# Kernel tuning notes

Hardware: AMD Instinct MI355X
Metric: run time of the kernel (lower is better)

## Reference

```python
import jax, jax.numpy as jnp
import numpy as np

D = 32   # input_dim == all hidden dims
L = 4    # number of GeneralizedRelationalConv layers
R = 36   # num_relation (incl. inverse relations)


def _bellmanford(edge_index, edge_type, h_index, r_index, num_nodes,
                 query_emb, rel_W, rel_b, conv_W, conv_b):
    """NBFNet Bellman-Ford pass: relation-conditioned conv with PNA aggregation."""
    B = r_index.shape[0]
    N = num_nodes
    E = edge_type.shape[0]
    d = query_emb.shape[1]

    query = query_emb[r_index]                                   # [B, d]
    # boundary condition: indicator embedding at the head node
    boundary = jnp.zeros((B, N, d), jnp.float32).at[jnp.arange(B), h_index].add(query)

    src, dst = edge_index[0], edge_index[1]
    # augment every node with a self-loop carrying the boundary message
    idx_aug = jnp.concatenate([dst, jnp.arange(N)])              # [E + N]
    deg = jax.ops.segment_sum(jnp.ones(E + N, jnp.float32), idx_aug, num_segments=N)  # >= 1
    dlog = jnp.log(deg)
    scale = dlog / jnp.mean(dlog)
    # PNA degree scalers: identity / amplification / attenuation
    scales = jnp.stack([jnp.ones_like(scale), scale, 1.0 / jnp.clip(scale, 1e-2)], axis=-1)  # [N, 3]

    x = boundary
    for l in range(L):
        # dependent relation embeddings: linear projection of the query
        rel = (query @ rel_W[l].T + rel_b[l]).reshape(B, R, d)   # [B, R, d]
        # distmult message: gather source state, modulate by edge relation
        msg = x[:, src, :] * rel[:, edge_type, :]                # [B, E, d]
        msg = jnp.concatenate([msg, boundary], axis=1)           # [B, E+N, d] incl. self-loops

        def agg(m):  # segment stats over destination nodes
            s = jax.ops.segment_sum(m, idx_aug, num_segments=N)
            sq = jax.ops.segment_sum(m * m, idx_aug, num_segments=N)
            mx = jax.ops.segment_max(m, idx_aug, num_segments=N)
            mn = jax.ops.segment_min(m, idx_aug, num_segments=N)
            return s, sq, mx, mn

        s, sq, mx, mn = jax.vmap(agg)(msg)                       # each [B, N, d]
        mean = s / deg[:, None]
        sq_mean = sq / deg[:, None]
        std = jnp.sqrt(jnp.clip(sq_mean - mean * mean, 1e-6))
        feats = jnp.stack([mean, mx, mn, std], axis=-1).reshape(B, N, 4 * d)
        update = (feats[..., None] * scales[None, :, None, :]).reshape(B, N, 12 * d)
        # combine: linear over cat(input, pna_update) then ReLU
        x = jax.nn.relu(jnp.concatenate([x, update], axis=-1) @ conv_W[l].T + conv_b[l])

    node_query = jnp.broadcast_to(query[:, None, :], (B, N, d))
    return jnp.concatenate([x, node_query], axis=-1)             # [B, N, 2d]


def setup_inputs() -> dict:
    key = jax.random.key(0)
    ks = jax.random.split(key, 10)
    N, E, B, K = 20000, 200000, 4, 32
    return {
        "edge_index": jax.random.randint(ks[0], (2, E), 0, N),
        "edge_type": jax.random.randint(ks[1], (E,), 0, R),
        "h_index": jax.random.randint(ks[2], (B,), 0, N),
        "t_index": jax.random.randint(ks[3], (B, K), 0, N),
        "r_index": jax.random.randint(ks[4], (B,), 0, R),
        "num_nodes": N,
        "query_emb": jax.random.normal(ks[5], (R, D), jnp.float32) * 0.1,
        "rel_W": jax.random.normal(ks[6], (L, R * D, D), jnp.float32) * 0.1,
        "rel_b": jnp.zeros((L, R * D), jnp.float32),
        "conv_W": jax.random.normal(ks[7], (L, D, 13 * D), jnp.float32) * 0.05,
        "conv_b": jnp.zeros((L, D), jnp.float32),
        "mlp_W1": jax.random.normal(ks[8], (2 * D, 2 * D), jnp.float32) * 0.1,
        "mlp_b1": jnp.zeros((2 * D,), jnp.float32),
        "mlp_W2": jax.random.normal(ks[9], (1, 2 * D), jnp.float32) * 0.1,
        "mlp_b2": jnp.zeros((1,), jnp.float32),
    }


def reference(edge_index, edge_type, h_index, t_index, r_index, num_nodes,
              query_emb, rel_W, rel_b, conv_W, conv_b,
              mlp_W1, mlp_b1, mlp_W2, mlp_b2):
    feature = _bellmanford(edge_index, edge_type, h_index, r_index, num_nodes,
                           query_emb, rel_W, rel_b, conv_W, conv_b)
    B = h_index.shape[0]
    f_t = feature[jnp.arange(B)[:, None], t_index]               # [B, K, 2d]
    h = jax.nn.relu(f_t @ mlp_W1.T + mlp_b1)
    score = (h @ mlp_W2.T + mlp_b2)[..., 0]                      # [B, K]
    return score
```

## Files before the change

kernel.cpp:

```cpp
#include <hip/hip_runtime.h>
#include <hip/hip_bf16.h>

#define N_NODES 20000
#define N_EDGES 200000
#define BB 4
#define KK 32
#define DD 32
#define RR 36
#define LL 4
#define NCHUNKS (N_NODES / 16)
#define NBLK 79

constexpr size_t OFF_X0   = 0;
constexpr size_t OFF_X1   = OFF_X0 + (size_t)BB * N_NODES * DD;
constexpr size_t OFF_RP   = OFF_X1 + (size_t)BB * N_NODES * DD;
constexpr size_t OFF_CUR  = OFF_RP + 20032;
constexpr size_t OFF_ES   = OFF_CUR + N_NODES;
constexpr size_t OFF_DEG  = OFF_ES + N_EDGES;
constexpr size_t OFF_SC   = OFF_DEG + N_NODES;
constexpr size_t OFF_INV  = OFF_SC + N_NODES;
constexpr size_t OFF_BS   = OFF_INV + N_NODES;
constexpr size_t OFF_BL   = OFF_BS + 128;
constexpr size_t OFF_BO   = OFF_BL + 128;
constexpr size_t OFF_MEAN = OFF_BO + 128;
constexpr size_t OFF_REL  = OFF_MEAN + 16;
constexpr size_t OFF_PW   = OFF_REL + (size_t)LL * RR * BB * DD;
constexpr size_t OFF_F    = OFF_PW + (size_t)LL * 4 * 3328;


__global__ void k_init(const int* __restrict__ h_index, const int* __restrict__ r_index,
                       const float* __restrict__ query_emb, float* __restrict__ x0,
                       int* __restrict__ cursor) {
    int i = blockIdx.x * blockDim.x + threadIdx.x;
    int stride = gridDim.x * blockDim.x;
    for (int t = i; t < N_NODES; t += stride) cursor[t] = 0;
    for (int t = i; t < BB * N_NODES * DD; t += stride) {
        int b = t & 3; int d = (t >> 2) & 31; int n = t >> 7;
        float v = 0.f;
        if (n == h_index[b]) v = query_emb[r_index[b] * DD + d];
        x0[t] = v;
    }
}

__global__ void k_hist(const int* __restrict__ ei, int* __restrict__ cursor) {
    int e = blockIdx.x * blockDim.x + threadIdx.x;
    if (e < N_EDGES) atomicAdd(&cursor[ei[N_EDGES + e]], 1);
}

__global__ void k_part(const int* __restrict__ cursor, int* __restrict__ bsum,
                       float* __restrict__ blog) {
    __shared__ int si[256];
    __shared__ float sf2[256];
    int tid = threadIdx.x;
    int i = blockIdx.x * 256 + tid;
    int v = (i < N_NODES) ? cursor[i] : 0;
    float lg = (i < N_NODES) ? logf((float)(v + 1)) : 0.f;
    si[tid] = v; sf2[tid] = lg;
    __syncthreads();
    for (int off = 128; off > 0; off >>= 1) {
        if (tid < off) { si[tid] += si[tid + off]; sf2[tid] += sf2[tid + off]; }
        __syncthreads();
    }
    if (tid == 0) { bsum[blockIdx.x] = si[0]; blog[blockIdx.x] = sf2[0]; }
}

__global__ void k_scan2(const int* __restrict__ bsum, const float* __restrict__ blog,
                        int* __restrict__ boff, float* __restrict__ meanw) {
    __shared__ int si[128];
    __shared__ float sf2[128];
    int t = threadIdx.x;
    int v = (t < NBLK) ? bsum[t] : 0;
    float lg = (t < NBLK) ? blog[t] : 0.f;
    si[t] = v; sf2[t] = lg;
    __syncthreads();
    for (int off = 1; off < 128; off <<= 1) {
        int tv = (t >= off) ? si[t - off] : 0;
        float tf = (t >= off) ? sf2[t - off] : 0.f;
        __syncthreads();
        si[t] += tv; sf2[t] += tf;
        __syncthreads();
    }
    if (t < NBLK) boff[t] = si[t] - v;
    if (t == 127) meanw[0] = sf2[127] / (float)N_NODES;
}

__global__ void k_final(int* __restrict__ cursor, int* __restrict__ row_ptr,
                        const int* __restrict__ boff, const float* __restrict__ meanw,
                        float* __restrict__ rdeg, float* __restrict__ scale,
                        float* __restrict__ invs) {
    __shared__ int si[256];
    int tid = threadIdx.x;
    int i = blockIdx.x * 256 + tid;
    int v = (i < N_NODES) ? cursor[i] : 0;
    si[tid] = v;
    __syncthreads();
    for (int off = 1; off < 256; off <<= 1) {
        int tv = (tid >= off) ? si[tid - off] : 0;
        __syncthreads();
        si[tid] += tv;
        __syncthreads();
    }
    int rp = boff[blockIdx.x] + si[tid] - v;
    if (i < N_NODES) {
        row_ptr[i] = rp;
        cursor[i] = rp;
        float dg = (float)(v + 1);
        float sc = logf(dg) / meanw[0];
        rdeg[i] = 1.f / dg;
        scale[i] = sc;
        invs[i] = 1.f / fmaxf(sc, 0.01f);
    }
    if (i == 0) row_ptr[N_NODES] = N_EDGES;
}

__global__ void k_scatter(const int* __restrict__ ei, const int* __restrict__ et,
                          int* __restrict__ cursor, int* __restrict__ es) {
    int e = blockIdx.x * blockDim.x + threadIdx.x;
    if (e < N_EDGES) {
        int dnode = ei[N_EDGES + e];
        int p = atomicAdd(&cursor[dnode], 1);
        es[p] = ei[e] | (et[e] << 16);
    }
}

__global__ void k_prep_w(const float* __restrict__ query_emb, const int* __restrict__ r_index,
                         const float* __restrict__ rel_W, const float* __restrict__ rel_b,
                         const float* __restrict__ conv_W,
                         float* __restrict__ rel_all, float* __restrict__ pw) {
    int i = blockIdx.x * blockDim.x + threadIdx.x;
    const int NREL = LL * BB * RR * DD;
    if (i < NREL) {
        int d = i & 31;
        int ty = (i >> 5) % RR;
        int b = (i / (32 * RR)) & 3;
        int l = i / (32 * RR * BB);
        const float* q = query_emb + r_index[b] * DD;
        const float* w = rel_W + ((size_t)l * RR * DD + ty * DD + d) * DD;
        float acc = rel_b[l * RR * DD + ty * DD + d];
        #pragma unroll
        for (int k2 = 0; k2 < DD; ++k2) acc = fmaf(q[k2], w[k2], acc);
        rel_all[(((size_t)l * RR + ty) * DD + d) * BB + b] = acc;
    } else {
        int i2 = i - NREL;
        if (i2 >= LL * 4 * 3328) return;
        int r = i2 % 3328; int lg2 = i2 / 3328;
        int og = lg2 & 3, l = lg2 >> 2;
        int o, col;
        if (r < 256) { col = r >> 3; o = og * 8 + (r & 7); }
        else {
            int r2 = r - 256;
            int jj = r2 / 96, rem = r2 % 96;
            int pf = rem >> 3;
            o = og * 8 + (rem & 7);
            col = DD + (jj * 4 + pf / 3) * 3 + (pf % 3);
        }
        pw[i2] = conv_W[(size_t)(l * DD + o) * (13 * DD) + col];
    }
}

__launch_bounds__(256, 6)
__global__ void k_gather(const float* __restrict__ xin, float4* __restrict__ Fq,
                         const int* __restrict__ row_ptr, const int* __restrict__ es,
                         const float* __restrict__ rel_l, const float* __restrict__ rdeg,
                         const int* __restrict__ h_index, const int* __restrict__ r_index,
                         const float* __restrict__ query_emb) {
    __shared__ __align__(16) float s_rel[RR * BB * DD];
    const int tid = threadIdx.x;
    {
        const float4* p4 = (const float4*)rel_l;
        float4* s4 = (float4*)s_rel;
        for (int i = tid; i < RR * BB * DD / 4; i += 256) s4[i] = p4[i];
    }
    const int lane = tid & 63;
    const int d = lane & 31;
    const int par = lane >> 5;
    int hb[4]; float qv[4];
    #pragma unroll
    for (int b = 0; b < 4; ++b) {
        hb[b] = h_index[b];
        qv[b] = query_emb[r_index[b] * DD + d];
    }
    __syncthreads();

    const int nwaves = gridDim.x * 4;
    for (int n = blockIdx.x * 4 + (tid >> 6); n < N_NODES; n += nwaves) {
        float sa[4], sq[4], mx[4], mn[4];
        #pragma unroll
        for (int b = 0; b < 4; ++b) {
            float bv = (n == hb[b]) ? qv[b] : 0.f;
            float bs = par ? 0.f : bv;
            sa[b] = bs; sq[b] = bs * bv; mx[b] = bv; mn[b] = bv;
        }
        auto proc = [&](int ee) {
            int pk = es[ee];
            float4 xv = *(const float4*)(xin + ((size_t)(pk & 0xFFFF) * DD + d) * 4);
            float4 rv = *(const float4*)(s_rel + (((pk >> 16) * DD) + d) * 4);
            #pragma unroll
            for (int b = 0; b < 4; ++b) {
                float m = (&xv.x)[b] * (&rv.x)[b];
                sa[b] += m; sq[b] = fmaf(m, m, sq[b]);
                mx[b] = fmaxf(mx[b], m); mn[b] = fminf(mn[b], m);
            }
        };
        int e0 = row_ptr[n], e1 = row_ptr[n + 1];
        int e = e0 + par;
        for (; e + 6 < e1; e += 8) { proc(e); proc(e + 2); proc(e + 4); proc(e + 6); }
        for (; e < e1; e += 2) proc(e);
        #pragma unroll
        for (int b = 0; b < 4; ++b) {
            sa[b] += __shfl_xor(sa[b], 32);
            sq[b] += __shfl_xor(sq[b], 32);
            mx[b] = fmaxf(mx[b], __shfl_xor(mx[b], 32));
            mn[b] = fminf(mn[b], __shfl_xor(mn[b], 32));
        }
        float rd_ = rdeg[n];
        float mean[4], sd[4];
        #pragma unroll
        for (int b = 0; b < 4; ++b) {
            mean[b] = sa[b] * rd_;
            float sm = sq[b] * rd_;
            sd[b] = sqrtf(fmaxf(sm - mean[b] * mean[b], 1e-6f));
        }
        const int chunk = n >> 4, nl = n & 15;
        int tA = nl * 4 + par * 2;
        float4 fA, fB;
        fA.x = par ? mean[2] : mean[0]; fA.y = par ? mx[2] : mx[0];
        fA.z = par ? mn[2] : mn[0];     fA.w = par ? sd[2] : sd[0];
        fB.x = par ? mean[3] : mean[1]; fB.y = par ? mx[3] : mx[1];
        fB.z = par ? mn[3] : mn[1];     fB.w = par ? sd[3] : sd[1];
        Fq[(size_t)(chunk * 32 + d) * 64 + tA] = fA;
        Fq[(size_t)(chunk * 32 + d) * 64 + tA + 1] = fB;
    }
}

__launch_bounds__(256, 6)
__global__ void k_conv(const float* __restrict__ xin, float* __restrict__ xout,
                       const float4* __restrict__ Fq, const float* __restrict__ pw_l,
                       const float* __restrict__ scale, const float* __restrict__ invs,
                       const float* __restrict__ conv_b_l) {
    const int tid = threadIdx.x;
    const int og = __builtin_amdgcn_readfirstlane(tid >> 6);
    const int lane = tid & 63;
    const int chunk = blockIdx.x;
    const float* wxp = pw_l + og * 3328;
    const float* wfp = wxp + 256;

    const int nl2 = lane >> 2, b2 = lane & 3;
    const int n = chunk * 16 + nl2;

    float y0[8], y1[8], y2[8];
    #pragma unroll
    for (int oo = 0; oo < 8; ++oo) {
        y0[oo] = conv_b_l[og * 8 + oo];
        y1[oo] = 0.f;
        y2[oo] = 0.f;
    }

    const float* xb = xin + (size_t)n * 128 + b2;
    #pragma unroll 2
    for (int jg = 0; jg < 8; ++jg) {
        float cxv[4];
        #pragma unroll
        for (int dj = 0; dj < 4; ++dj) cxv[dj] = xb[(jg * 4 + dj) * 4];
        #pragma unroll
        for (int dj = 0; dj < 4; ++dj) {
            const float* wp = wxp + (jg * 4 + dj) * 8;
            #pragma unroll
            for (int oo = 0; oo < 8; ++oo) y0[oo] = fmaf(cxv[dj], wp[oo], y0[oo]);
        }
    }

    float4 fa = Fq[(size_t)(chunk * 32) * 64 + lane];
    #pragma unroll 1
    for (int jj = 0; jj < 32; ++jj) {
        float4 fb = Fq[(size_t)(chunk * 32 + jj + 1) * 64 + lane];
        const float* wp = wfp + jj * 96;
        #pragma unroll
        for (int f = 0; f < 4; ++f) {
            float cv = (&fa.x)[f];
            const float* w8 = wp + f * 24;
            #pragma unroll
            for (int oo = 0; oo < 8; ++oo) y0[oo] = fmaf(cv, w8[oo], y0[oo]);
            #pragma unroll
            for (int oo = 0; oo < 8; ++oo) y1[oo] = fmaf(cv, w8[8 + oo], y1[oo]);
            #pragma unroll
            for (int oo = 0; oo < 8; ++oo) y2[oo] = fmaf(cv, w8[16 + oo], y2[oo]);
        }
        fa = fb;
    }

    float scn = scale[n], ivn = invs[n];
    float* xo = xout + (size_t)n * 128 + b2;
    #pragma unroll
    for (int oo = 0; oo < 8; ++oo) {
        float v = fmaxf(0.f, y0[oo] + scn * y1[oo] + ivn * y2[oo]);
        xo[(og * 8 + oo) * 4] = v;
    }
}

__global__ void k_score(const float* __restrict__ xL, const float* __restrict__ query_emb,
                        const int* __restrict__ r_index, const int* __restrict__ t_index,
                        const float* __restrict__ W1, const float* __restrict__ b1,
                        const float* __restrict__ W2, const float* __restrict__ b2,
                        float* __restrict__ out) {
    int bi = blockIdx.x;
    int b = bi >> 5, kk = bi & 31;
    int j = threadIdx.x;
    __shared__ float sf[64];
    int t = t_index[b * KK + kk];
    float f = (j < DD) ? xL[(size_t)t * 128 + j * 4 + b]
                       : query_emb[r_index[b] * DD + (j - DD)];
    sf[j] = f;
    __syncthreads();
    float acc = b1[j];
    #pragma unroll 8
    for (int i2 = 0; i2 < 64; ++i2) acc = fmaf(sf[i2], W1[j * 64 + i2], acc);
    float h = fmaxf(acc, 0.f);
    float prod = h * W2[j];
    #pragma unroll
    for (int off = 32; off > 0; off >>= 1) prod += __shfl_down(prod, off);
    if (j == 0) out[b * KK + kk] = prod + b2[0];
}

extern "C" void kernel_launch(void* const* d_in, const int* in_sizes, int n_in,
                              void* d_out, int out_size, void* d_ws, size_t ws_size,
                              hipStream_t stream) {
    const int* ei        = (const int*)d_in[0];
    const int* et        = (const int*)d_in[1];
    const int* h_index   = (const int*)d_in[2];
    const int* t_index   = (const int*)d_in[3];
    const int* r_index   = (const int*)d_in[4];
    const float* query_emb = (const float*)d_in[6];
    const float* rel_W   = (const float*)d_in[7];
    const float* rel_b   = (const float*)d_in[8];
    const float* conv_W  = (const float*)d_in[9];
    const float* conv_b  = (const float*)d_in[10];
    const float* W1      = (const float*)d_in[11];
    const float* b1      = (const float*)d_in[12];
    const float* W2      = (const float*)d_in[13];
    const float* b2      = (const float*)d_in[14];

    float* ws = (float*)d_ws;
    float* x0      = ws + OFF_X0;
    float* x1      = ws + OFF_X1;
    int*   row_ptr = (int*)(ws + OFF_RP);
    int*   cursor  = (int*)(ws + OFF_CUR);
    int*   es      = (int*)(ws + OFF_ES);
    float* rdeg    = ws + OFF_DEG;
    float* sc      = ws + OFF_SC;
    float* invs    = ws + OFF_INV;
    int*   bsum    = (int*)(ws + OFF_BS);
    float* blog    = ws + OFF_BL;
    int*   boff    = (int*)(ws + OFF_BO);
    float* meanw   = ws + OFF_MEAN;
    float* rel_all = ws + OFF_REL;
    float* pw      = ws + OFF_PW;
    float4* Fq     = (float4*)(ws + OFF_F);
    float* out     = (float*)d_out;

    k_init<<<1024, 256, 0, stream>>>(h_index, r_index, query_emb, x0, cursor);
    k_hist<<<(N_EDGES + 255) / 256, 256, 0, stream>>>(ei, cursor);
    k_part<<<NBLK, 256, 0, stream>>>(cursor, bsum, blog);
    k_scan2<<<1, 128, 0, stream>>>(bsum, blog, boff, meanw);
    k_final<<<NBLK, 256, 0, stream>>>(cursor, row_ptr, boff, meanw, rdeg, sc, invs);
    k_scatter<<<(N_EDGES + 255) / 256, 256, 0, stream>>>(ei, et, cursor, es);
    const int NPREP = LL * BB * RR * DD + LL * 4 * 3328;
    k_prep_w<<<(NPREP + 255) / 256, 256, 0, stream>>>(query_emb, r_index, rel_W, rel_b,
                                                      conv_W, rel_all, pw);

    for (int l = 0; l < LL; ++l) {
        const float* xi = (l & 1) ? x1 : x0;
        float* xo = (l & 1) ? x0 : x1;
        k_gather<<<1536, 256, 0, stream>>>(xi, Fq, row_ptr, es,
                                           rel_all + (size_t)l * RR * BB * DD,
                                           rdeg, h_index, r_index, query_emb);
        k_conv<<<NCHUNKS, 256, 0, stream>>>(xi, xo, Fq, pw + (size_t)l * 4 * 3328,
                                            sc, invs, conv_b + l * DD);
    }

    k_score<<<BB * KK, 64, 0, stream>>>(x0, query_emb, r_index, t_index, W1, b1, W2, b2, out);
}
```

Baseline: 267.0 us.

## Fuse gather and conv kernels per layer via shared-memory feature tile

Merges the per-layer aggregation kernel and the dense conv kernel into one kernel where each block aggregates 16 nodes, stores their PNA features in a swizzled shared-memory tile, and then applies the conv projection. This drops the global Fq round trip and one launch per layer. In exchange it uses 1250 blocks with a fixed 16 nodes each, no longer grid-strided, adds 32KB of extra LDS and lowers the occupancy hint, and imbalanced node degrees now stall the whole block at the barrier.

```diff
diff --git a/kernel.cpp b/kernel.cpp
--- a/kernel.cpp
+++ b/kernel.cpp
@@ -25,7 +25,6 @@
 constexpr size_t OFF_MEAN = OFF_BO + 128;
 constexpr size_t OFF_REL  = OFF_MEAN + 16;
 constexpr size_t OFF_PW   = OFF_REL + (size_t)LL * RR * BB * DD;
-constexpr size_t OFF_F    = OFF_PW + (size_t)LL * 4 * 3328;
 
 
 __global__ void k_init(const int* __restrict__ h_index, const int* __restrict__ r_index,
@@ -158,22 +157,27 @@
     }
 }
 
-__launch_bounds__(256, 6)
-__global__ void k_gather(const float* __restrict__ xin, float4* __restrict__ Fq,
-                         const int* __restrict__ row_ptr, const int* __restrict__ es,
-                         const float* __restrict__ rel_l, const float* __restrict__ rdeg,
-                         const int* __restrict__ h_index, const int* __restrict__ r_index,
-                         const float* __restrict__ query_emb) {
+__launch_bounds__(256, 3)
+__global__ void k_layer(const float* __restrict__ xin, float* __restrict__ xout,
+                        const int* __restrict__ row_ptr, const int* __restrict__ es,
+                        const float* __restrict__ rel_l, const float* __restrict__ pw_l,
+                        const float* __restrict__ rdeg, const float* __restrict__ scale,
+                        const float* __restrict__ invs,
+                        const int* __restrict__ h_index, const int* __restrict__ r_index,
+                        const float* __restrict__ query_emb, const float* __restrict__ conv_b_l) {
     __shared__ __align__(16) float s_rel[RR * BB * DD];
+    __shared__ __align__(16) float4 s_F[64 * 32];
     const int tid = threadIdx.x;
     {
         const float4* p4 = (const float4*)rel_l;
         float4* s4 = (float4*)s_rel;
         for (int i = tid; i < RR * BB * DD / 4; i += 256) s4[i] = p4[i];
     }
+    const int wv = tid >> 6;
     const int lane = tid & 63;
     const int d = lane & 31;
     const int par = lane >> 5;
+    const int chunk = blockIdx.x;
     int hb[4]; float qv[4];
     #pragma unroll
     for (int b = 0; b < 4; ++b) {
@@ -182,8 +186,10 @@
     }
     __syncthreads();
 
-    const int nwaves = gridDim.x * 4;
-    for (int n = blockIdx.x * 4 + (tid >> 6); n < N_NODES; n += nwaves) {
+    #pragma unroll 1
+    for (int i4 = 0; i4 < 4; ++i4) {
+        const int nl = wv * 4 + i4;
+        const int n = chunk * 16 + nl;
         float sa[4], sq[4], mx[4], mn[4];
         #pragma unroll
         for (int b = 0; b < 4; ++b) {
@@ -221,80 +227,71 @@
             float sm = sq[b] * rd_;
             sd[b] = sqrtf(fmaxf(sm - mean[b] * mean[b], 1e-6f));
         }
-        const int chunk = n >> 4, nl = n & 15;
         int tA = nl * 4 + par * 2;
         float4 fA, fB;
         fA.x = par ? mean[2] : mean[0]; fA.y = par ? mx[2] : mx[0];
         fA.z = par ? mn[2] : mn[0];     fA.w = par ? sd[2] : sd[0];
         fB.x = par ? mean[3] : mean[1]; fB.y = par ? mx[3] : mx[1];
         fB.z = par ? mn[3] : mn[1];     fB.w = par ? sd[3] : sd[1];
-        Fq[(size_t)(chunk * 32 + d) * 64 + tA] = fA;
-        Fq[(size_t)(chunk * 32 + d) * 64 + tA + 1] = fB;
-    }
-}
-
-__launch_bounds__(256, 6)
-__global__ void k_conv(const float* __restrict__ xin, float* __restrict__ xout,
-                       const float4* __restrict__ Fq, const float* __restrict__ pw_l,
-                       const float* __restrict__ scale, const float* __restrict__ invs,
-                       const float* __restrict__ conv_b_l) {
-    const int tid = threadIdx.x;
-    const int og = __builtin_amdgcn_readfirstlane(tid >> 6);
-    const int lane = tid & 63;
-    const int chunk = blockIdx.x;
-    const float* wxp = pw_l + og * 3328;
-    const float* wfp = wxp + 256;
-
-    const int nl2 = lane >> 2, b2 = lane & 3;
-    const int n = chunk * 16 + nl2;
-
-    float y0[8], y1[8], y2[8];
-    #pragma unroll
-    for (int oo = 0; oo < 8; ++oo) {
-        y0[oo] = conv_b_l[og * 8 + oo];
-        y1[oo] = 0.f;
-        y2[oo] = 0.f;
-    }
-
-    const float* xb = xin + (size_t)n * 128 + b2;
-    #pragma unroll 2
-    for (int jg = 0; jg < 8; ++jg) {
-        float cxv[4];
-        #pragma unroll
-        for (int dj = 0; dj < 4; ++dj) cxv[dj] = xb[(jg * 4 + dj) * 4];
-        #pragma unroll
-        for (int dj = 0; dj < 4; ++dj) {
-            const float* wp = wxp + (jg * 4 + dj) * 8;
+        s_F[tA * 32 + (d ^ (tA & 7))] = fA;
+        s_F[(tA + 1) * 32 + (d ^ ((tA + 1) & 7))] = fB;
+    }
+    __syncthreads();
+
+    {
+        const int og = __builtin_amdgcn_readfirstlane(wv);
+        const float* wxp = pw_l + og * 3328;
+        const float* wfp = wxp + 256;
+        const int nl2 = lane >> 2, b2 = lane & 3;
+        const int n = chunk * 16 + nl2;
+        const int sw = lane & 7;
+
+        float y0[8], y1[8], y2[8];
+        #pragma unroll
+        for (int oo = 0; oo < 8; ++oo) {
+            y0[oo] = conv_b_l[og * 8 + oo];
+            y1[oo] = 0.f;
+            y2[oo] = 0.f;
+        }
+
+        const float* xb = xin + (size_t)n * 128 + b2;
+        #pragma unroll 2
+        for (int jg = 0; jg < 8; ++jg) {
+            float cxv[4];
             #pragma unroll
-            for (int oo = 0; oo < 8; ++oo) y0[oo] = fmaf(cxv[dj], wp[oo], y0[oo]);
-        }
-    }
-
-    float4 fa = Fq[(size_t)(chunk * 32) * 64 + lane];
-    #pragma unroll 1
-    for (int jj = 0; jj < 32; ++jj) {
-        float4 fb = Fq[(size_t)(chunk * 32 + jj + 1) * 64 + lane];
-        const float* wp = wfp + jj * 96;
-        #pragma unroll
-        for (int f = 0; f < 4; ++f) {
-            float cv = (&fa.x)[f];
-            const float* w8 = wp + f * 24;
+            for (int dj = 0; dj < 4; ++dj) cxv[dj] = xb[(jg * 4 + dj) * 4];
             #pragma unroll
-            for (int oo = 0; oo < 8; ++oo) y0[oo] = fmaf(cv, w8[oo], y0[oo]);
+            for (int dj = 0; dj < 4; ++dj) {
+                const float* wp = wxp + (jg * 4 + dj) * 8;
+                #pragma unroll
+                for (int oo = 0; oo < 8; ++oo) y0[oo] = fmaf(cxv[dj], wp[oo], y0[oo]);
+            }
+        }
+
+        #pragma unroll 1
+        for (int jj = 0; jj < 32; ++jj) {
+            float4 cf = s_F[lane * 32 + (jj ^ sw)];
+            const float* wp = wfp + jj * 96;
             #pragma unroll
-            for (int oo = 0; oo < 8; ++oo) y1[oo] = fmaf(cv, w8[8 + oo], y1[oo]);
-            #pragma unroll
-            for (int oo = 0; oo < 8; ++oo) y2[oo] = fmaf(cv, w8[16 + oo], y2[oo]);
-        }
-        fa = fb;
-    }
-
-    float scn = scale[n], ivn = invs[n];
-    float* xo = xout + (size_t)n * 128 + b2;
-    #pragma unroll
-    for (int oo = 0; oo < 8; ++oo) {
-        float v = fmaxf(0.f, y0[oo] + scn * y1[oo] + ivn * y2[oo]);
-        xo[(og * 8 + oo) * 4] = v;
+            for (int f = 0; f < 4; ++f) {
+                float cv = (&cf.x)[f];
+                const float* w8 = wp + f * 24;
+                #pragma unroll
+                for (int oo = 0; oo < 8; ++oo) y0[oo] = fmaf(cv, w8[oo], y0[oo]);
+                #pragma unroll
+                for (int oo = 0; oo < 8; ++oo) y1[oo] = fmaf(cv, w8[8 + oo], y1[oo]);
+                #pragma unroll
+                for (int oo = 0; oo < 8; ++oo) y2[oo] = fmaf(cv, w8[16 + oo], y2[oo]);
+            }
+        }
+
+        float scn = scale[n], ivn = invs[n];
+        float* xo = xout + (size_t)n * 128 + b2;
+        #pragma unroll
+        for (int oo = 0; oo < 8; ++oo) {
+            float v = fmaxf(0.f, y0[oo] + scn * y1[oo] + ivn * y2[oo]);
+            xo[(og * 8 + oo) * 4] = v;
+        }
     }
 }
 
@@ -355,7 +352,6 @@
     float* meanw   = ws + OFF_MEAN;
     float* rel_all = ws + OFF_REL;
     float* pw      = ws + OFF_PW;
-    float4* Fq     = (float4*)(ws + OFF_F);
     float* out     = (float*)d_out;
 
     k_init<<<1024, 256, 0, stream>>>(h_index, r_index, query_emb, x0, cursor);
@@ -371,11 +367,11 @@
     for (int l = 0; l < LL; ++l) {
         const float* xi = (l & 1) ? x1 : x0;
         float* xo = (l & 1) ? x0 : x1;
-        k_gather<<<1536, 256, 0, stream>>>(xi, Fq, row_ptr, es,
-                                           rel_all + (size_t)l * RR * BB * DD,
-                                           rdeg, h_index, r_index, query_emb);
-        k_conv<<<NCHUNKS, 256, 0, stream>>>(xi, xo, Fq, pw + (size_t)l * 4 * 3328,
-                                            sc, invs, conv_b + l * DD);
+        k_layer<<<NCHUNKS, 256, 0, stream>>>(xi, xo, row_ptr, es,
+                                             rel_all + (size_t)l * RR * BB * DD,
+                                             pw + (size_t)l * 4 * 3328,
+                                             rdeg, sc, invs, h_index, r_index,
+                                             query_emb, conv_b + l * DD);
     }
 
     k_score<<<BB * KK, 64, 0, stream>>>(x0, query_emb, r_index, t_index, W1, b1, W2, b2, out);
```

Measured after the change: 310.5 us. 16.3% more time.
